# Optimization experiments

Hardware: AMD Instinct MI355X
Metric: run time of the kernel (lower is better)

## Reference

```python
import jax, jax.numpy as jnp
import numpy as np

CROP = 48
THRESHOLD = 0.5
IOU_THRESHOLD = 0.5


def _conv(x, w, b):
    # x: [N,H,W,C], w: [kh,kw,Cin,Cout]
    y = jax.lax.conv_general_dilated(x, w, (1, 1), 'VALID',
                                     dimension_numbers=('NHWC', 'HWIO', 'NHWC'))
    return y + b


def _prelu(x, a):
    # a broadcasts over the channel-last axis
    return jnp.where(x >= 0, x, a * x)


def _maxpool(x, k, s, p):
    return jax.lax.reduce_window(x, -jnp.inf, jax.lax.max,
                                 (1, k, k, 1), (1, s, s, 1),
                                 ((0, 0), (p, p), (p, p), (0, 0)))


def _nms_keep(boxes, scores, valid, iou_thr):
    # fixed-shape greedy NMS (torchvision semantics: suppress iou > thr)
    N = boxes.shape[0]
    s = jnp.where(valid, scores, -jnp.inf)
    order = jnp.argsort(-s)
    b = boxes[order]
    x1, y1, x2, y2 = b[:, 0], b[:, 1], b[:, 2], b[:, 3]
    area = (x2 - x1) * (y2 - y1)
    xx1 = jnp.maximum(x1[:, None], x1[None, :])
    yy1 = jnp.maximum(y1[:, None], y1[None, :])
    xx2 = jnp.minimum(x2[:, None], x2[None, :])
    yy2 = jnp.minimum(y2[:, None], y2[None, :])
    inter = jnp.clip(xx2 - xx1, 0.0) * jnp.clip(yy2 - yy1, 0.0)
    iou = inter / (area[:, None] + area[None, :] - inter + 1e-12)
    keep0 = valid[order]
    idx = jnp.arange(N)

    def body(i, keep):
        sup = (iou[i] > iou_thr) & (idx > i) & keep[i] & keep
        return keep & ~sup

    keep_sorted = jax.lax.fori_loop(0, N, body, keep0)
    return jnp.zeros(N, bool).at[order].set(keep_sorted)


def setup_inputs() -> dict:
    key = jax.random.key(0)
    ks = jax.random.split(key, 24)
    H = W = 1024
    N = 2048
    image = jax.random.uniform(ks[0], (H, W, 3), jnp.float32) * 255.0
    x1 = jax.random.uniform(ks[1], (N,), jnp.float32) * (W - 130)
    y1 = jax.random.uniform(ks[2], (N,), jnp.float32) * (H - 130)
    bw = 20.0 + jax.random.uniform(ks[3], (N,), jnp.float32) * 100.0
    bh = 20.0 + jax.random.uniform(ks[4], (N,), jnp.float32) * 100.0
    bboxes = jnp.stack([x1, y1, x1 + bw, y1 + bh], axis=1)
    rn = lambda k, sh, s: jax.random.normal(k, sh, jnp.float32) * s
    return {
        'bboxes': bboxes, 'image': image,
        'conv1_w': rn(ks[5], (3, 3, 3, 32), 0.05), 'conv1_b': rn(ks[6], (32,), 0.01),
        'prelu1': 0.25 * jnp.ones((32,), jnp.float32),
        'conv2_w': rn(ks[7], (3, 3, 32, 64), 0.05), 'conv2_b': rn(ks[8], (64,), 0.01),
        'prelu2': 0.25 * jnp.ones((64,), jnp.float32),
        'conv3_w': rn(ks[9], (3, 3, 64, 64), 0.05), 'conv3_b': rn(ks[10], (64,), 0.01),
        'prelu3': 0.25 * jnp.ones((64,), jnp.float32),
        'conv4_w': rn(ks[11], (2, 2, 64, 128), 0.05), 'conv4_b': rn(ks[12], (128,), 0.01),
        'prelu4': 0.25 * jnp.ones((128,), jnp.float32),
        'fc5_w': rn(ks[13], (256, 1152), 0.02), 'fc5_b': rn(ks[14], (256,), 0.01),
        'prelu5': 0.25 * jnp.ones((256,), jnp.float32),
        'fc6a_w': rn(ks[15], (2, 256), 0.1), 'fc6a_b': rn(ks[16], (2,), 0.01),
        'fc6b_w': rn(ks[17], (4, 256), 0.1), 'fc6b_b': rn(ks[18], (4,), 0.01),
    }


def reference(bboxes, image, conv1_w, conv1_b, prelu1, conv2_w, conv2_b, prelu2,
              conv3_w, conv3_b, prelu3, conv4_w, conv4_b, prelu4,
              fc5_w, fc5_b, prelu5, fc6a_w, fc6a_b, fc6b_w, fc6b_b):
    H, W = image.shape[0], image.shape[1]
    N = bboxes.shape[0]
    # preprocess (torch: (x - 127.5) * 0.0078125)
    data = (image - 127.5) * 0.0078125  # [H,W,3]
    # clip boxes in place like the torch forward
    bx1 = jnp.clip(bboxes[:, 0], 0.0, None)
    by1 = jnp.clip(bboxes[:, 1], 0.0, None)
    bx2 = jnp.clip(bboxes[:, 2], None, float(W))
    by2 = jnp.clip(bboxes[:, 3], None, float(H))
    bb = jnp.stack([bx1, by1, bx2, by2], axis=1)  # clipped boxes [N,4]
    # integer crop windows (torch .int() truncation; coords >= 0)
    ib = bb.astype(jnp.int32)
    cw = jnp.maximum(ib[:, 2] - ib[:, 0], 1)
    ch = jnp.maximum(ib[:, 3] - ib[:, 1], 1)
    # nearest-neighbor resize to 48x48 (F.interpolate default mode='nearest')
    r = jnp.arange(CROP, dtype=jnp.int32)
    xs = ib[:, 0:1] + (r[None, :] * cw[:, None]) // CROP  # [N,48]
    ys = ib[:, 1:2] + (r[None, :] * ch[:, None]) // CROP  # [N,48]
    crops = data[ys[:, :, None], xs[:, None, :], :]  # [N,48,48,3] gather
    # CNN trunk
    h = _maxpool(_prelu(_conv(crops, conv1_w, conv1_b), prelu1), 3, 2, 1)
    h = _maxpool(_prelu(_conv(h, conv2_w, conv2_b), prelu2), 3, 2, 0)
    h = _maxpool(_prelu(_conv(h, conv3_w, conv3_b), prelu3), 2, 2, 0)
    h = _prelu(_conv(h, conv4_w, conv4_b), prelu4)  # [N,3,3,128]
    h = jnp.transpose(h, (0, 3, 1, 2)).reshape(N, -1)  # NCHW flatten like torch -> [N,1152]
    h = _prelu(h @ fc5_w.T + fc5_b, prelu5)  # [N,256]
    cls = jax.nn.softmax(h @ fc6a_w.T + fc6a_b, axis=1)  # [N,2]
    reg = h @ fc6b_w.T + fc6b_b  # [N,4]
    score = cls[:, 1]
    valid = score >= THRESHOLD
    w = bb[:, 2] - bb[:, 0]
    hgt = bb[:, 3] - bb[:, 1]
    out = jnp.stack([bb[:, 0] + reg[:, 0] * w,
                     bb[:, 1] + reg[:, 1] * hgt,
                     bb[:, 2] + reg[:, 2] * w,
                     bb[:, 3] + reg[:, 3] * hgt], axis=1)  # [N,4]
    keep = _nms_keep(out, score, valid, IOU_THRESHOLD)
    return jnp.where(keep[:, None], out, 0.0)
```

## Files before the change

kernel.cpp:

```cpp
#include <hip/hip_runtime.h>
#include <math.h>
#include <stdint.h>

#define NBOX 2048

#define P1_RS 25
#define P1_CS 576
#define P1_SZ 18432

__device__ __forceinline__ void fma4(float4& a, float s, const float4& w) {
  a.x = fmaf(s, w.x, a.x); a.y = fmaf(s, w.y, a.y);
  a.z = fmaf(s, w.z, a.z); a.w = fmaf(s, w.w, a.w);
}
__device__ __forceinline__ float4 max4(float4 a, float4 b) {
  return make_float4(fmaxf(a.x,b.x), fmaxf(a.y,b.y), fmaxf(a.z,b.z), fmaxf(a.w,b.w));
}
__device__ __forceinline__ float4 max34(float4 a, float4 b, float4 c) {
  return max4(max4(a, b), c);
}
__device__ __forceinline__ float4 prelu4(float4 v, float4 a) {
  float4 r;
  r.x = v.x >= 0.f ? v.x : a.x*v.x;
  r.y = v.y >= 0.f ? v.y : a.y*v.y;
  r.z = v.z >= 0.f ? v.z : a.z*v.z;
  r.w = v.w >= 0.f ? v.w : a.w*v.w;
  return r;
}
__device__ __forceinline__ float4 shfl4(float4 v, int src) {
  float4 r;
  r.x = __shfl(v.x, src, 64); r.y = __shfl(v.y, src, 64);
  r.z = __shfl(v.z, src, 64); r.w = __shfl(v.w, src, 64);
  return r;
}

__global__ __launch_bounds__(256) void k1_crop_conv1(
    const float* __restrict__ bboxes, const float* __restrict__ image,
    const float* __restrict__ w1, const float* __restrict__ b1, const float* __restrict__ a1,
    float* __restrict__ p1ws, int box0)
{
  __shared__ float crop[48*48*3];
  const int tid = threadIdx.x;
  const int n = box0 + blockIdx.x;

  float f0 = bboxes[n*4+0], f1 = bboxes[n*4+1], f2 = bboxes[n*4+2], f3 = bboxes[n*4+3];
  float bx1 = fmaxf(f0, 0.f), by1 = fmaxf(f1, 0.f);
  float bx2 = fminf(f2, 1024.f), by2 = fminf(f3, 1024.f);
  int ix1 = (int)bx1, iy1 = (int)by1, ix2 = (int)bx2, iy2 = (int)by2;
  int cw = ix2 - ix1; if (cw < 1) cw = 1;
  int ch = iy2 - iy1; if (ch < 1) ch = 1;

  for (int idx = tid; idx < 6912; idx += 256) {
    int c = idx % 3; int t = idx / 3; int j = t % 48; int i = t / 48;
    int gx = ix1 + (j * cw) / 48;
    int gy = iy1 + (i * ch) / 48;
    float v = image[(gy*1024 + gx)*3 + c];
    crop[idx] = (v - 127.5f) * 0.0078125f;
  }
  __syncthreads();

  float* p1o = p1ws + (size_t)blockIdx.x * P1_SZ;

  for (int slot = tid; slot < 1104; slot += 256) {
    int cq = slot & 7;
    int t2 = slot >> 3;
    int pjq = t2 % 6;
    int pi  = t2 / 6;
    int pj0 = pjq * 4;
    int c0 = 2*pj0 - 1;
    float4 bias  = *(const float4*)&b1[cq*4];
    float4 alpha = *(const float4*)&a1[cq*4];
    float4 mx[4];
#pragma unroll
    for (int t = 0; t < 4; t++) mx[t] = make_float4(-3.0e38f,-3.0e38f,-3.0e38f,-3.0e38f);

#pragma unroll
    for (int dr = 0; dr < 3; dr++) {
      int r = 2*pi - 1 + dr;
      if (r < 0 || r > 45) continue;
      float4 acc[9];
#pragma unroll
      for (int c = 0; c < 9; c++) acc[c] = bias;
#pragma unroll
      for (int kh = 0; kh < 3; kh++) {
        int row = r + kh;
        float s[33];
#pragma unroll
        for (int d = 0; d < 11; d++) {
          int cc = c0 + d; cc = cc < 0 ? 0 : (cc > 47 ? 47 : cc);
          int base = row*144 + cc*3;
          s[d*3+0] = crop[base+0];
          s[d*3+1] = crop[base+1];
          s[d*3+2] = crop[base+2];
        }
#pragma unroll
        for (int kw = 0; kw < 3; kw++) {
#pragma unroll
          for (int ci = 0; ci < 3; ci++) {
            float4 w = *(const float4*)&w1[((kh*3+kw)*3+ci)*32 + cq*4];
#pragma unroll
            for (int c = 0; c < 9; c++) fma4(acc[c], s[(c+kw)*3+ci], w);
          }
        }
      }
#pragma unroll
      for (int c = 0; c < 9; c++) {
        int cabs = c0 + c;
        if (cabs < 0 || cabs > 45) continue;
        float4 pv = prelu4(acc[c], alpha);
#pragma unroll
        for (int t = 0; t < 4; t++) {
          if (c >= 2*t && c <= 2*t+2) mx[t] = max4(mx[t], pv);
        }
      }
    }
#pragma unroll
    for (int t = 0; t < 4; t++) {
      int pj = pj0 + t;
      if (pj < 23) {
        int base = pi*P1_RS + pj;
        p1o[(cq*4+0)*P1_CS + base] = mx[t].x;
        p1o[(cq*4+1)*P1_CS + base] = mx[t].y;
        p1o[(cq*4+2)*P1_CS + base] = mx[t].z;
        p1o[(cq*4+3)*P1_CS + base] = mx[t].w;
      }
    }
  }
}

#define K2_LOADW(W, CI, KH) { \
  const float* wp_ = w2 + (((KH)*3)*32 + (CI))*64 + co0; \
  W[0] = *(const float4*)(wp_);            W[1] = *(const float4*)(wp_ + 4); \
  W[2] = *(const float4*)(wp_ + 2048);     W[3] = *(const float4*)(wp_ + 2052); \
  W[4] = *(const float4*)(wp_ + 4096);     W[5] = *(const float4*)(wp_ + 4100); }

#define K2_COMP(W, CIL, KH) { \
  const float* ip_ = &in_s[(CIL)*P1_CS + (rl+(KH))*P1_RS + j0]; \
  float s_[9]; \
  _Pragma("unroll") for (int d_ = 0; d_ < 9; d_++) s_[d_] = ip_[d_]; \
  _Pragma("unroll") for (int kw_ = 0; kw_ < 3; kw_++) { \
    _Pragma("unroll") for (int jj_ = 0; jj_ < 7; jj_++) { \
      fma4(acc[jj_][0], s_[jj_+kw_], W[kw_*2]); \
      fma4(acc[jj_][1], s_[jj_+kw_], W[kw_*2+1]); } } }

#define K2_STORE8(PJ, LO, HI) { \
  float* d_ = p2o + (size_t)co0*120 + pi*12 + (PJ); \
  float4 lo_ = (LO), hi_ = (HI); \
  d_[0]   = lo_.x; d_[120] = lo_.y; d_[240] = lo_.z; d_[360] = lo_.w; \
  d_[480] = hi_.x; d_[600] = hi_.y; d_[720] = hi_.z; d_[840] = hi_.w; }

__global__ __launch_bounds__(512, 4) void k2_conv2(
    const float* __restrict__ w2, const float* __restrict__ b2, const float* __restrict__ a2,
    const float* __restrict__ p1ws, float* __restrict__ p2ws)
{
  __shared__ float in_s[9216];
  const int tid = threadIdx.x;
  const float* p1o = p1ws + (size_t)blockIdx.x * P1_SZ;
  float* p2o = p2ws + (size_t)blockIdx.x * 7680;

  const int wav = __builtin_amdgcn_readfirstlane(tid >> 6);
  const int lane = tid & 63;
  int jt = lane / 21;
  int rl = lane - jt * 21;
  if (lane == 63) { jt = 2; rl = 20; }
  const int j0 = jt * 7;
  const int co0 = wav * 8;

  float4 bL = *(const float4*)&b2[co0];
  float4 bH = *(const float4*)&b2[co0+4];
  float4 aL = *(const float4*)&a2[co0];
  float4 aH = *(const float4*)&a2[co0+4];

  float4 acc[7][2];
#pragma unroll
  for (int jj = 0; jj < 7; jj++) { acc[jj][0] = bL; acc[jj][1] = bH; }

#pragma unroll 1
  for (int h = 0; h < 2; h++) {
    __syncthreads();
    for (int i4 = tid; i4 < 2304; i4 += 512)
      *(float4*)&in_s[i4*4] = *(const float4*)&p1o[h*9216 + i4*4];
    __syncthreads();

    const int cb = h*16;
    float4 wA[6], wB[6];
    K2_LOADW(wA, cb+0, 0);
#pragma unroll 1
    for (int ci = 0; ci < 16; ci += 2) {
      K2_LOADW(wB, cb+ci, 1);
      K2_COMP(wA, ci, 0);
      K2_LOADW(wA, cb+ci, 2);
      K2_COMP(wB, ci, 1);
      K2_LOADW(wB, cb+ci+1, 0);
      K2_COMP(wA, ci, 2);
      K2_LOADW(wA, cb+ci+1, 1);
      K2_COMP(wB, ci+1, 0);
      K2_LOADW(wB, cb+ci+1, 2);
      K2_COMP(wA, ci+1, 1);
      if (ci + 2 < 16) K2_LOADW(wA, cb+ci+2, 0);
      K2_COMP(wB, ci+1, 2);
    }
  }

#pragma unroll
  for (int jj = 0; jj < 7; jj++) {
    acc[jj][0] = prelu4(acc[jj][0], aL);
    acc[jj][1] = prelu4(acc[jj][1], aH);
  }

#pragma unroll
  for (int jj = 0; jj < 7; jj++) {
#pragma unroll
    for (int h = 0; h < 2; h++) {
      float4 v = acc[jj][h];
      float4 d1 = shfl4(v, lane + 1);
      float4 d2 = shfl4(v, lane + 2);
      acc[jj][h] = max34(v, d1, d2);
    }
  }
  float4 r0[2], r1[2];
#pragma unroll
  for (int h = 0; h < 2; h++) {
    r0[h] = shfl4(acc[0][h], lane + 21);
    r1[h] = shfl4(acc[1][h], lane + 21);
  }

  if (((rl & 1) == 0) && rl <= 18) {
    const int pi = rl >> 1;
    if (jt == 0) {
      K2_STORE8(0, max34(acc[0][0],acc[1][0],acc[2][0]), max34(acc[0][1],acc[1][1],acc[2][1]));
      K2_STORE8(1, max34(acc[2][0],acc[3][0],acc[4][0]), max34(acc[2][1],acc[3][1],acc[4][1]));
      K2_STORE8(2, max34(acc[4][0],acc[5][0],acc[6][0]), max34(acc[4][1],acc[5][1],acc[6][1]));
      K2_STORE8(3, max34(acc[6][0],r0[0],r1[0]),          max34(acc[6][1],r0[1],r1[1]));
    } else if (jt == 1) {
      K2_STORE8(4, max34(acc[1][0],acc[2][0],acc[3][0]), max34(acc[1][1],acc[2][1],acc[3][1]));
      K2_STORE8(5, max34(acc[3][0],acc[4][0],acc[5][0]), max34(acc[3][1],acc[4][1],acc[5][1]));
      K2_STORE8(6, max34(acc[5][0],acc[6][0],r0[0]),     max34(acc[5][1],acc[6][1],r0[1]));
    } else {
      K2_STORE8(7, max34(acc[0][0],acc[1][0],acc[2][0]), max34(acc[0][1],acc[1][1],acc[2][1]));
      K2_STORE8(8, max34(acc[2][0],acc[3][0],acc[4][0]), max34(acc[2][1],acc[3][1],acc[4][1]));
      K2_STORE8(9, max34(acc[4][0],acc[5][0],acc[6][0]), max34(acc[4][1],acc[5][1],acc[6][1]));
    }
  }
}

#define K3_LOADW(W, CI, KH) { \
  const float* wp_ = w3 + (((KH)*3)*64 + (CI))*64 + co0; \
  W[0] = *(const float4*)(wp_);            W[1] = *(const float4*)(wp_ + 4); \
  W[2] = *(const float4*)(wp_ + 4096);     W[3] = *(const float4*)(wp_ + 4100); \
  W[4] = *(const float4*)(wp_ + 8192);     W[5] = *(const float4*)(wp_ + 8196); }

#define K3_COMP(W, CIL, KH) { \
  const float* ip_ = ibase + (CIL)*120 + (KH)*12; \
  float2 sA_ = *(const float2*)(ip_); \
  float2 sB_ = *(const float2*)(ip_ + 2); \
  float s_[4] = {sA_.x, sA_.y, sB_.x, sB_.y}; \
  _Pragma("unroll") for (int kw_ = 0; kw_ < 3; kw_++) { \
    _Pragma("unroll") for (int c_ = 0; c_ < 2; c_++) { \
      fma4(acc[c_][0], s_[c_+kw_], W[kw_*2]); \
      fma4(acc[c_][1], s_[c_+kw_], W[kw_*2+1]); } } }

__global__ __launch_bounds__(512, 4) void k3_conv3(
    const float* __restrict__ w3, const float* __restrict__ b3, const float* __restrict__ a3,
    const float* __restrict__ p2ws, float* __restrict__ p3ws)
{
  __shared__ float in_s[7696];
  const int tid = threadIdx.x;
  const float* p2o = p2ws + (size_t)(blockIdx.x*2) * 7680;
  float* p3o0 = p3ws + (size_t)(blockIdx.x*2) * 1024;

  const int wav = __builtin_amdgcn_readfirstlane(tid >> 6);
  const int lane = tid & 63;
  const int b  = lane >> 5;
  const int r  = (lane >> 2) & 7;
  const int cg = lane & 3;
  const int co0 = wav * 8;

  float4 bL = *(const float4*)&b3[co0];
  float4 bH = *(const float4*)&b3[co0+4];
  float4 aL = *(const float4*)&a3[co0];
  float4 aH = *(const float4*)&a3[co0+4];

  float4 acc[2][2];
  acc[0][0] = bL; acc[0][1] = bH; acc[1][0] = bL; acc[1][1] = bH;

  const float* ibase = &in_s[b*3848 + r*12 + cg*2];

#pragma unroll 1
  for (int h = 0; h < 2; h++) {
    __syncthreads();
    for (int i4 = tid; i4 < 1920; i4 += 512) {
      int bb = (i4 >= 960) ? 1 : 0;
      int k = i4 - bb*960;
      *(float4*)&in_s[bb*3848 + k*4] = *(const float4*)&p2o[(size_t)bb*7680 + h*3840 + k*4];
    }
    __syncthreads();

    const int cb = h*32;
    float4 wA[6], wB[6];
    K3_LOADW(wA, cb+0, 0);
#pragma unroll 1
    for (int ci = 0; ci < 32; ci += 2) {
      K3_LOADW(wB, cb+ci, 1);
      K3_COMP(wA, ci, 0);
      K3_LOADW(wA, cb+ci, 2);
      K3_COMP(wB, ci, 1);
      K3_LOADW(wB, cb+ci+1, 0);
      K3_COMP(wA, ci, 2);
      K3_LOADW(wA, cb+ci+1, 1);
      K3_COMP(wB, ci+1, 0);
      K3_LOADW(wB, cb+ci+1, 2);
      K3_COMP(wA, ci+1, 1);
      if (ci + 2 < 32) K3_LOADW(wA, cb+ci+2, 0);
      K3_COMP(wB, ci+1, 2);
    }
  }

  float4 hm[2];
#pragma unroll
  for (int h = 0; h < 2; h++) {
    float4 p0 = prelu4(acc[0][h], h ? aH : aL);
    float4 p1 = prelu4(acc[1][h], h ? aH : aL);
    hm[h] = max4(p0, p1);
  }
  float4 o[2];
#pragma unroll
  for (int h = 0; h < 2; h++) {
    float4 d = shfl4(hm[h], lane + 4);
    o[h] = max4(hm[h], d);
  }
  if ((r & 1) == 0) {
    const int pi = r >> 1;
    float* d = p3o0 + b*1024 + (size_t)co0*16 + pi*4 + cg;
    d[0]   = o[0].x; d[16]  = o[0].y; d[32]  = o[0].z; d[48]  = o[0].w;
    d[64]  = o[1].x; d[80]  = o[1].y; d[96]  = o[1].z; d[112] = o[1].w;
  }
}

#define K4_LOADW(W, CI) { \
  const float* wp_ = w4 + (CI)*128 + co0; \
  W[0] = *(const float4*)(wp_);           W[1] = *(const float4*)(wp_ + 4); \
  W[2] = *(const float4*)(wp_ + 8192);    W[3] = *(const float4*)(wp_ + 8196); \
  W[4] = *(const float4*)(wp_ + 16384);   W[5] = *(const float4*)(wp_ + 16388); \
  W[6] = *(const float4*)(wp_ + 24576);   W[7] = *(const float4*)(wp_ + 24580); }

#define K4_COMP(W, CI) { \
  const float* ip_ = base + (CI)*16; \
  float i00 = ip_[0], i01 = ip_[1], i10 = ip_[4], i11 = ip_[5]; \
  fma4(acc0, i00, W[0]); fma4(acc1, i00, W[1]); \
  fma4(acc0, i01, W[2]); fma4(acc1, i01, W[3]); \
  fma4(acc0, i10, W[4]); fma4(acc1, i10, W[5]); \
  fma4(acc0, i11, W[6]); fma4(acc1, i11, W[7]); }

__global__ __launch_bounds__(512) void k4_conv4(
    const float* __restrict__ w4, const float* __restrict__ b4, const float* __restrict__ a4,
    const float* __restrict__ p3ws, float* __restrict__ c4ws)
{
  __shared__ float p3s[4*1032];
  const int tid = threadIdx.x;
  const int bi0 = blockIdx.x * 4;

  for (int i4 = tid; i4 < 1024; i4 += 512) {
    int bb = i4 >> 8, k = i4 & 255;
    *(float4*)&p3s[bb*1032 + k*4] = *(const float4*)&p3ws[(size_t)(bi0+bb)*1024 + k*4];
  }
  __syncthreads();

  const int wav = __builtin_amdgcn_readfirstlane(tid >> 6);
  const int lane = tid & 63;
  const int bx = lane >> 4;
  const int sp = lane & 15;
  const bool act = sp < 9;
  const int sq = act ? sp : 8;
  const int r = sq / 3, c = sq - 3*r;
  const float* base = &p3s[bx*1032 + r*4 + c];
  float* c4o = c4ws + (size_t)(bi0+bx)*1152;

#pragma unroll 1
  for (int p = 0; p < 2; p++) {
    const int co0 = p*64 + wav*8;
    float4 bL = *(const float4*)&b4[co0];
    float4 bH = *(const float4*)&b4[co0+4];
    float4 aL = *(const float4*)&a4[co0];
    float4 aH = *(const float4*)&a4[co0+4];
    float4 acc0 = bL, acc1 = bH;

    float4 wA[8], wB[8];
    K4_LOADW(wA, 0);
#pragma unroll 1
    for (int ci = 0; ci < 64; ci += 2) {
      K4_LOADW(wB, ci+1);
      K4_COMP(wA, ci);
      if (ci + 2 < 64) K4_LOADW(wA, ci+2);
      K4_COMP(wB, ci+1);
    }

    if (act) {
      float4 p0 = prelu4(acc0, aL);
      float4 p1 = prelu4(acc1, aH);
      float* d = c4o + (size_t)co0*9 + sp;
      d[0]  = p0.x; d[9]  = p0.y; d[18] = p0.z; d[27] = p0.w;
      d[36] = p1.x; d[45] = p1.y; d[54] = p1.z; d[63] = p1.w;
    }
  }
}

__global__ __launch_bounds__(512) void k5_fc(
    const float* __restrict__ fc5w, const float* __restrict__ fc5b, const float* __restrict__ a5,
    const float* __restrict__ w6a, const float* __restrict__ b6a,
    const float* __restrict__ w6b, const float* __restrict__ b6b,
    const float* __restrict__ bboxes, const float* __restrict__ c4ws,
    float* __restrict__ ws_scores, float* __restrict__ ws_boxes, int box0)
{
  __shared__ float c4s[8*1152];
  __shared__ float hs[8*256];
  __shared__ float l6[8][6];
  const int tid = threadIdx.x;
  const int lb0 = blockIdx.x * 8;
  for (int idx4 = tid; idx4 < 2304; idx4 += 512)
    *(float4*)&c4s[idx4*4] = *(const float4*)&c4ws[(size_t)lb0*1152 + idx4*4];
  __syncthreads();

  const int wav = __builtin_amdgcn_readfirstlane(tid >> 6);
  const int lane = tid & 63;
  const int half = lane >> 5;
  const int l32  = lane & 31;
  const int b    = 2*(wav & 3) + half;
  const int ob   = (wav >> 2) * 128;
  const float* cb = &c4s[b*1152 + l32*4];

#pragma unroll 1
  for (int oi = 0; oi < 128; oi++) {
    const int o = ob + oi;
    const float* wr = fc5w + (size_t)o*1152 + l32*4;
    float acc = 0.f;
#pragma unroll
    for (int j = 0; j < 9; j++) {
      float4 wv = *(const float4*)(wr + j*128);
      float4 cv = *(const float4*)(cb + j*128);
      acc = fmaf(cv.x, wv.x, acc);
      acc = fmaf(cv.y, wv.y, acc);
      acc = fmaf(cv.z, wv.z, acc);
      acc = fmaf(cv.w, wv.w, acc);
    }
    acc += __shfl_down(acc, 16, 32);
    acc += __shfl_down(acc,  8, 32);
    acc += __shfl_down(acc,  4, 32);
    acc += __shfl_down(acc,  2, 32);
    acc += __shfl_down(acc,  1, 32);
    if (l32 == 0) {
      float h = acc + fc5b[o];
      h = h >= 0.f ? h : a5[o]*h;
      hs[b*256 + o] = h;
    }
  }
  __syncthreads();

  if (tid < 48) {
    int bb = tid / 6, oi = tid % 6;
    const float* w = (oi < 2) ? &w6a[oi*256] : &w6b[(oi-2)*256];
    float d = (oi < 2) ? b6a[oi] : b6b[oi-2];
    const float* hh = &hs[bb*256];
    for (int k = 0; k < 256; k++) d += hh[k]*w[k];
    l6[bb][oi] = d;
  }
  __syncthreads();
  if (tid < 8) {
    int n = box0 + lb0 + tid;
    float l0 = l6[tid][0], l1 = l6[tid][1];
    float m = fmaxf(l0, l1);
    float e0 = expf(l0-m), e1 = expf(l1-m);
    float score = e1/(e0+e1);
    float r0 = l6[tid][2], r1 = l6[tid][3], r2 = l6[tid][4], r3 = l6[tid][5];
    float f0 = bboxes[n*4+0], f1 = bboxes[n*4+1], f2 = bboxes[n*4+2], f3 = bboxes[n*4+3];
    float bx1 = fmaxf(f0, 0.f), by1 = fmaxf(f1, 0.f);
    float bx2 = fminf(f2, 1024.f), by2 = fminf(f3, 1024.f);
    float w_ = bx2-bx1, h_ = by2-by1;
    ws_scores[n] = score;
    float4 ob2 = make_float4(bx1 + r0*w_, by1 + r1*h_, bx2 + r2*w_, by2 + r3*h_);
    *(float4*)&ws_boxes[n*4] = ob2;
  }
}

__global__ __launch_bounds__(1024) void k6a_sort(
    const float* __restrict__ ws_scores, const float* __restrict__ ws_boxes,
    int* __restrict__ sidx_ws, float* __restrict__ sbox_ws,
    float* __restrict__ area_ws, int* __restrict__ nv_ws)
{
  __shared__ float skey[2048];
  __shared__ int   sidx[2048];
  const int tid = threadIdx.x;
  for (int i = tid; i < 2048; i += 1024) {
    float s = ws_scores[i];
    skey[i] = (s >= 0.5f) ? s : -INFINITY;
    sidx[i] = i;
  }
  __syncthreads();
  for (int k = 2; k <= 2048; k <<= 1) {
    for (int j = k >> 1; j > 0; j >>= 1) {
      for (int i = tid; i < 2048; i += 1024) {
        int ixj = i ^ j;
        if (ixj > i) {
          float a = skey[i], b = skey[ixj];
          int ia = sidx[i], ib = sidx[ixj];
          bool up = ((i & k) == 0);
          bool aAfterB = (a < b) || (a == b && ia > ib);
          if (up ? aAfterB : !aAfterB) {
            skey[i] = b; skey[ixj] = a; sidx[i] = ib; sidx[ixj] = ia;
          }
        }
      }
      __syncthreads();
    }
  }
  if (tid == 0) nv_ws[0] = 2048;
  __syncthreads();
  for (int i = tid; i < 2048; i += 1024) {
    if (skey[i] == -INFINITY && (i == 0 || skey[i-1] != -INFINITY)) nv_ws[0] = i;
    int n = sidx[i];
    sidx_ws[i] = n;
    float4 b = *(const float4*)&ws_boxes[n*4];
    *(float4*)&sbox_ws[i*4] = b;
    area_ws[i] = (b.z-b.x)*(b.w-b.y);
  }
}

__global__ __launch_bounds__(256) void k6b_iou(
    const int* __restrict__ nv_ws, const float* __restrict__ sbox_ws,
    const float* __restrict__ area_ws, unsigned long long* __restrict__ M)
{
  const int nv = nv_ws[0];
  int gt = blockIdx.x*256 + threadIdx.x;
  for (int w = gt; w < 2048*32; w += 128*256) {
    int i = w >> 5, wg = w & 31;
    if (i >= nv) continue;
    float4 bi = *(const float4*)&sbox_ws[i*4];
    float ai = area_ws[i];
    unsigned long long m = 0;
    int jbase = wg*64;
    if (jbase + 63 > i) {
      for (int jj = 0; jj < 64; jj++) {
        int j = jbase + jj;
        if (j <= i) continue;
        float4 bj = *(const float4*)&sbox_ws[j*4];
        float xx1 = fmaxf(bi.x, bj.x), yy1 = fmaxf(bi.y, bj.y);
        float xx2 = fminf(bi.z, bj.z), yy2 = fminf(bi.w, bj.w);
        float iw = fmaxf(xx2-xx1, 0.f), ih = fmaxf(yy2-yy1, 0.f);
        float inter = iw*ih;
        float iou = inter / (ai + area_ws[j] - inter + 1e-12f);
        if (iou > 0.5f) m |= (1ull << jj);
      }
    }
    M[w] = m;
  }
}

__global__ __launch_bounds__(1024) void k6c_scan(
    const int* __restrict__ nv_ws, const int* __restrict__ sidx_ws,
    const float* __restrict__ sbox_ws, const unsigned long long* __restrict__ M,
    float* __restrict__ out)
{
  __shared__ unsigned long long Msh[128*32];
  __shared__ unsigned long long rem_sh[32];
  const int tid = threadIdx.x;
  const int nv = nv_ws[0];
  unsigned long long rem = 0;

  for (int c0 = 0; c0 < 2048; c0 += 128) {
    if (c0 >= nv) break;
    for (int w = tid; w < 128*32; w += 1024) {
      int i = c0 + (w >> 5);
      if (i < nv) Msh[w] = M[(size_t)i*32 + (w & 31)];
    }
    __syncthreads();
    if (tid < 64) {
      int iend = c0 + 128; if (iend > nv) iend = nv;
      for (int i = c0; i < iend; i += 4) {
        unsigned long long m0=0, m1=0, m2=0, m3=0;
        int base = (i - c0) << 5;
        if (tid < 32) {
          m0 = Msh[base + tid];
          if (i+1 < iend) m1 = Msh[base + 32 + tid];
          if (i+2 < iend) m2 = Msh[base + 64 + tid];
          if (i+3 < iend) m3 = Msh[base + 96 + tid];
        }
        unsigned long long rw = __shfl(rem, (i >> 6), 64);
        if (!((rw >> (i & 63)) & 1ull)) rem |= m0;
        if (i+1 < iend) {
          rw = __shfl(rem, ((i+1) >> 6), 64);
          if (!((rw >> ((i+1) & 63)) & 1ull)) rem |= m1;
        }
        if (i+2 < iend) {
          rw = __shfl(rem, ((i+2) >> 6), 64);
          if (!((rw >> ((i+2) & 63)) & 1ull)) rem |= m2;
        }
        if (i+3 < iend) {
          rw = __shfl(rem, ((i+3) >> 6), 64);
          if (!((rw >> ((i+3) & 63)) & 1ull)) rem |= m3;
        }
      }
    }
    __syncthreads();
  }
  if (tid < 32) rem_sh[tid] = rem;
  __syncthreads();
  for (int i = tid; i < 2048; i += 1024) {
    bool keep = (i < nv) && !((rem_sh[i >> 6] >> (i & 63)) & 1ull);
    int n = sidx_ws[i];
    float4 b = *(const float4*)&sbox_ws[i*4];
    float4 o = keep ? b : make_float4(0.f,0.f,0.f,0.f);
    *(float4*)&out[n*4] = o;
  }
}

extern "C" void kernel_launch(void* const* d_in, const int* in_sizes, int n_in,
                              void* d_out, int out_size, void* d_ws, size_t ws_size,
                              hipStream_t stream)
{
  const float* bboxes = (const float*)d_in[0];
  const float* image  = (const float*)d_in[1];
  const float* w1 = (const float*)d_in[2];  const float* b1 = (const float*)d_in[3];  const float* a1 = (const float*)d_in[4];
  const float* w2 = (const float*)d_in[5];  const float* b2 = (const float*)d_in[6];  const float* a2 = (const float*)d_in[7];
  const float* w3 = (const float*)d_in[8];  const float* b3 = (const float*)d_in[9];  const float* a3 = (const float*)d_in[10];
  const float* w4 = (const float*)d_in[11]; const float* b4 = (const float*)d_in[12]; const float* a4 = (const float*)d_in[13];
  const float* fc5w = (const float*)d_in[14]; const float* fc5b = (const float*)d_in[15]; const float* a5 = (const float*)d_in[16];
  const float* w6a = (const float*)d_in[17]; const float* b6a = (const float*)d_in[18];
  const float* w6b = (const float*)d_in[19]; const float* b6b = (const float*)d_in[20];
  float* out = (float*)d_out;

  char* ws = (char*)d_ws;
  size_t off = 0;
  auto alloc = [&](size_t bytes) -> size_t {
    size_t p = off; off += (bytes + 255) & ~(size_t)255; return p;
  };
  size_t o_scores = alloc(NBOX*4);
  size_t o_boxes  = alloc(NBOX*16);
  size_t o_sidx   = alloc(NBOX*4);
  size_t o_sbox   = alloc(NBOX*16);
  size_t o_area   = alloc(NBOX*4);
  size_t o_nv     = alloc(256);
  size_t o_M      = alloc((size_t)NBOX*32*8);
  size_t fixed = off;
  const size_t perbox = (size_t)(P1_SZ + 7680 + 1024 + 1152) * 4;

  int B = NBOX;
  if (fixed + (size_t)B*perbox > ws_size) {
    size_t avail = ws_size > fixed ? ws_size - fixed : 0;
    B = (int)(avail / perbox);
    B &= ~7;
    if (B < 8) B = 8;
    if (B > NBOX) B = NBOX;
  }
  size_t o_p1 = alloc((size_t)B*P1_SZ*4);
  size_t o_p2 = alloc((size_t)B*7680*4);
  size_t o_p3 = alloc((size_t)B*1024*4);
  size_t o_c4 = alloc((size_t)B*1152*4);

  float* ws_scores = (float*)(ws + o_scores);
  float* ws_boxes  = (float*)(ws + o_boxes);
  int*   sidxp     = (int*)(ws + o_sidx);
  float* sboxp     = (float*)(ws + o_sbox);
  float* areap     = (float*)(ws + o_area);
  int*   nvp       = (int*)(ws + o_nv);
  unsigned long long* Mp = (unsigned long long*)(ws + o_M);
  float* p1p = (float*)(ws + o_p1);
  float* p2p = (float*)(ws + o_p2);
  float* p3p = (float*)(ws + o_p3);
  float* c4p = (float*)(ws + o_c4);

  for (int c0 = 0; c0 < NBOX; c0 += B) {
    int Bc = NBOX - c0; if (Bc > B) Bc = B;
    k1_crop_conv1<<<Bc, 256, 0, stream>>>(bboxes, image, w1, b1, a1, p1p, c0);
    k2_conv2<<<Bc, 512, 0, stream>>>(w2, b2, a2, p1p, p2p);
    k3_conv3<<<Bc/2, 512, 0, stream>>>(w3, b3, a3, p2p, p3p);
    k4_conv4<<<Bc/4, 512, 0, stream>>>(w4, b4, a4, p3p, c4p);
    k5_fc<<<Bc/8, 512, 0, stream>>>(fc5w, fc5b, a5, w6a, b6a, w6b, b6b,
                                    bboxes, c4p, ws_scores, ws_boxes, c0);
  }
  k6a_sort<<<1, 1024, 0, stream>>>(ws_scores, ws_boxes, sidxp, sboxp, areap, nvp);
  k6b_iou<<<128, 256, 0, stream>>>(nvp, sboxp, areap, Mp);
  k6c_scan<<<1, 1024, 0, stream>>>(nvp, sidxp, sboxp, Mp, out);
}
```

Measured before the change: 1.552 ms.

## Fuse conv3 and conv4 kernels via shared memory, widen conv1 block, unroll fc5

Merges the conv3 and conv4 kernels so the pooled conv3 output stays in shared memory instead of round-tripping through a global workspace, and remaps conv4 work so each wave handles 32 output channels for one box. conv1 blocks grow to 512 threads, and the fc5 loop computes two outputs per iteration to reuse the activation loads. In exchange, the fused kernel drops the __launch_bounds__ occupancy hint and the conv4 weight prefetch double-buffering, and each block processes only 2 boxes in conv4 instead of 4.

```diff
diff --git a/kernel.cpp b/kernel.cpp
--- a/kernel.cpp
+++ b/kernel.cpp
@@ -33,7 +33,7 @@
   return r;
 }
 
-__global__ __launch_bounds__(256) void k1_crop_conv1(
+__global__ __launch_bounds__(512) void k1_crop_conv1(
     const float* __restrict__ bboxes, const float* __restrict__ image,
     const float* __restrict__ w1, const float* __restrict__ b1, const float* __restrict__ a1,
     float* __restrict__ p1ws, int box0)
@@ -49,7 +49,7 @@
   int cw = ix2 - ix1; if (cw < 1) cw = 1;
   int ch = iy2 - iy1; if (ch < 1) ch = 1;
 
-  for (int idx = tid; idx < 6912; idx += 256) {
+  for (int idx = tid; idx < 6912; idx += 512) {
     int c = idx % 3; int t = idx / 3; int j = t % 48; int i = t / 48;
     int gx = ix1 + (j * cw) / 48;
     int gy = iy1 + (i * ch) / 48;
@@ -60,7 +60,7 @@
 
   float* p1o = p1ws + (size_t)blockIdx.x * P1_SZ;
 
-  for (int slot = tid; slot < 1104; slot += 256) {
+  for (int slot = tid; slot < 1104; slot += 512) {
     int cq = slot & 7;
     int t2 = slot >> 3;
     int pjq = t2 % 6;
@@ -259,145 +259,120 @@
       fma4(acc[c_][0], s_[c_+kw_], W[kw_*2]); \
       fma4(acc[c_][1], s_[c_+kw_], W[kw_*2+1]); } } }
 
-__global__ __launch_bounds__(512, 4) void k3_conv3(
+__global__ __launch_bounds__(512) void k34_conv34(
     const float* __restrict__ w3, const float* __restrict__ b3, const float* __restrict__ a3,
-    const float* __restrict__ p2ws, float* __restrict__ p3ws)
+    const float* __restrict__ w4, const float* __restrict__ b4, const float* __restrict__ a4,
+    const float* __restrict__ p2ws, float* __restrict__ c4ws)
 {
   __shared__ float in_s[7696];
+  __shared__ float p3s[2*1032];
   const int tid = threadIdx.x;
-  const float* p2o = p2ws + (size_t)(blockIdx.x*2) * 7680;
-  float* p3o0 = p3ws + (size_t)(blockIdx.x*2) * 1024;
+  const int bi0 = blockIdx.x * 2;
+  const float* p2o = p2ws + (size_t)bi0 * 7680;
 
   const int wav = __builtin_amdgcn_readfirstlane(tid >> 6);
   const int lane = tid & 63;
-  const int b  = lane >> 5;
-  const int r  = (lane >> 2) & 7;
-  const int cg = lane & 3;
-  const int co0 = wav * 8;
-
-  float4 bL = *(const float4*)&b3[co0];
-  float4 bH = *(const float4*)&b3[co0+4];
-  float4 aL = *(const float4*)&a3[co0];
-  float4 aH = *(const float4*)&a3[co0+4];
-
-  float4 acc[2][2];
-  acc[0][0] = bL; acc[0][1] = bH; acc[1][0] = bL; acc[1][1] = bH;
-
-  const float* ibase = &in_s[b*3848 + r*12 + cg*2];
+
+  {
+    const int b  = lane >> 5;
+    const int r  = (lane >> 2) & 7;
+    const int cg = lane & 3;
+    const int co0 = wav * 8;
+
+    float4 bL = *(const float4*)&b3[co0];
+    float4 bH = *(const float4*)&b3[co0+4];
+    float4 aL = *(const float4*)&a3[co0];
+    float4 aH = *(const float4*)&a3[co0+4];
+
+    float4 acc[2][2];
+    acc[0][0] = bL; acc[0][1] = bH; acc[1][0] = bL; acc[1][1] = bH;
+
+    const float* ibase = &in_s[b*3848 + r*12 + cg*2];
 
 #pragma unroll 1
-  for (int h = 0; h < 2; h++) {
-    __syncthreads();
-    for (int i4 = tid; i4 < 1920; i4 += 512) {
-      int bb = (i4 >= 960) ? 1 : 0;
-      int k = i4 - bb*960;
-      *(float4*)&in_s[bb*3848 + k*4] = *(const float4*)&p2o[(size_t)bb*7680 + h*3840 + k*4];
-    }
-    __syncthreads();
-
-    const int cb = h*32;
-    float4 wA[6], wB[6];
-    K3_LOADW(wA, cb+0, 0);
+    for (int h = 0; h < 2; h++) {
+      __syncthreads();
+      for (int i4 = tid; i4 < 1920; i4 += 512) {
+        int bb = (i4 >= 960) ? 1 : 0;
+        int k = i4 - bb*960;
+        *(float4*)&in_s[bb*3848 + k*4] = *(const float4*)&p2o[(size_t)bb*7680 + h*3840 + k*4];
+      }
+      __syncthreads();
+
+      const int cb = h*32;
+      float4 wA[6], wB[6];
+      K3_LOADW(wA, cb+0, 0);
 #pragma unroll 1
-    for (int ci = 0; ci < 32; ci += 2) {
-      K3_LOADW(wB, cb+ci, 1);
-      K3_COMP(wA, ci, 0);
-      K3_LOADW(wA, cb+ci, 2);
-      K3_COMP(wB, ci, 1);
-      K3_LOADW(wB, cb+ci+1, 0);
-      K3_COMP(wA, ci, 2);
-      K3_LOADW(wA, cb+ci+1, 1);
-      K3_COMP(wB, ci+1, 0);
-      K3_LOADW(wB, cb+ci+1, 2);
-      K3_COMP(wA, ci+1, 1);
-      if (ci + 2 < 32) K3_LOADW(wA, cb+ci+2, 0);
-      K3_COMP(wB, ci+1, 2);
-    }
-  }
-
-  float4 hm[2];
-#pragma unroll
-  for (int h = 0; h < 2; h++) {
-    float4 p0 = prelu4(acc[0][h], h ? aH : aL);
-    float4 p1 = prelu4(acc[1][h], h ? aH : aL);
-    hm[h] = max4(p0, p1);
-  }
-  float4 o[2];
-#pragma unroll
-  for (int h = 0; h < 2; h++) {
-    float4 d = shfl4(hm[h], lane + 4);
-    o[h] = max4(hm[h], d);
-  }
-  if ((r & 1) == 0) {
-    const int pi = r >> 1;
-    float* d = p3o0 + b*1024 + (size_t)co0*16 + pi*4 + cg;
-    d[0]   = o[0].x; d[16]  = o[0].y; d[32]  = o[0].z; d[48]  = o[0].w;
-    d[64]  = o[1].x; d[80]  = o[1].y; d[96]  = o[1].z; d[112] = o[1].w;
-  }
-}
-
-#define K4_LOADW(W, CI) { \
-  const float* wp_ = w4 + (CI)*128 + co0; \
-  W[0] = *(const float4*)(wp_);           W[1] = *(const float4*)(wp_ + 4); \
-  W[2] = *(const float4*)(wp_ + 8192);    W[3] = *(const float4*)(wp_ + 8196); \
-  W[4] = *(const float4*)(wp_ + 16384);   W[5] = *(const float4*)(wp_ + 16388); \
-  W[6] = *(const float4*)(wp_ + 24576);   W[7] = *(const float4*)(wp_ + 24580); }
-
-#define K4_COMP(W, CI) { \
-  const float* ip_ = base + (CI)*16; \
-  float i00 = ip_[0], i01 = ip_[1], i10 = ip_[4], i11 = ip_[5]; \
-  fma4(acc0, i00, W[0]); fma4(acc1, i00, W[1]); \
-  fma4(acc0, i01, W[2]); fma4(acc1, i01, W[3]); \
-  fma4(acc0, i10, W[4]); fma4(acc1, i10, W[5]); \
-  fma4(acc0, i11, W[6]); fma4(acc1, i11, W[7]); }
-
-__global__ __launch_bounds__(512) void k4_conv4(
-    const float* __restrict__ w4, const float* __restrict__ b4, const float* __restrict__ a4,
-    const float* __restrict__ p3ws, float* __restrict__ c4ws)
-{
-  __shared__ float p3s[4*1032];
-  const int tid = threadIdx.x;
-  const int bi0 = blockIdx.x * 4;
-
-  for (int i4 = tid; i4 < 1024; i4 += 512) {
-    int bb = i4 >> 8, k = i4 & 255;
-    *(float4*)&p3s[bb*1032 + k*4] = *(const float4*)&p3ws[(size_t)(bi0+bb)*1024 + k*4];
-  }
-  __syncthreads();
-
-  const int wav = __builtin_amdgcn_readfirstlane(tid >> 6);
-  const int lane = tid & 63;
-  const int bx = lane >> 4;
-  const int sp = lane & 15;
-  const bool act = sp < 9;
-  const int sq = act ? sp : 8;
-  const int r = sq / 3, c = sq - 3*r;
-  const float* base = &p3s[bx*1032 + r*4 + c];
-  float* c4o = c4ws + (size_t)(bi0+bx)*1152;
-
+      for (int ci = 0; ci < 32; ci += 2) {
+        K3_LOADW(wB, cb+ci, 1);
+        K3_COMP(wA, ci, 0);
+        K3_LOADW(wA, cb+ci, 2);
+        K3_COMP(wB, ci, 1);
+        K3_LOADW(wB, cb+ci+1, 0);
+        K3_COMP(wA, ci, 2);
+        K3_LOADW(wA, cb+ci+1, 1);
+        K3_COMP(wB, ci+1, 0);
+        K3_LOADW(wB, cb+ci+1, 2);
+        K3_COMP(wA, ci+1, 1);
+        if (ci + 2 < 32) K3_LOADW(wA, cb+ci+2, 0);
+        K3_COMP(wB, ci+1, 2);
+      }
+    }
+
+    float4 hm[2];
+#pragma unroll
+    for (int h = 0; h < 2; h++) {
+      float4 p0 = prelu4(acc[0][h], h ? aH : aL);
+      float4 p1 = prelu4(acc[1][h], h ? aH : aL);
+      hm[h] = max4(p0, p1);
+    }
+    float4 o[2];
+#pragma unroll
+    for (int h = 0; h < 2; h++) {
+      float4 d = shfl4(hm[h], lane + 4);
+      o[h] = max4(hm[h], d);
+    }
+    if ((r & 1) == 0) {
+      const int pi = r >> 1;
+      float* d = &p3s[b*1032 + co0*16 + pi*4 + cg];
+      d[0]   = o[0].x; d[16]  = o[0].y; d[32]  = o[0].z; d[48]  = o[0].w;
+      d[64]  = o[1].x; d[80]  = o[1].y; d[96]  = o[1].z; d[112] = o[1].w;
+    }
+  }
+  __syncthreads();
+
+  {
+    const int bb  = wav >> 2;
+    const int wv  = wav & 3;
+    const int coq = lane >> 4;
+    const int sp  = lane & 15;
+    const bool act = sp < 9;
+    const int sq = act ? sp : 8;
+    const int r4 = sq / 3, cc4 = sq - 3*r4;
+    const int co8 = wv*32 + coq*8;
+    const float* base = &p3s[bb*1032 + r4*4 + cc4];
+    float* c4o = c4ws + (size_t)(bi0+bb)*1152;
+
+    float4 acc0 = *(const float4*)&b4[co8];
+    float4 acc1 = *(const float4*)&b4[co8+4];
 #pragma unroll 1
-  for (int p = 0; p < 2; p++) {
-    const int co0 = p*64 + wav*8;
-    float4 bL = *(const float4*)&b4[co0];
-    float4 bH = *(const float4*)&b4[co0+4];
-    float4 aL = *(const float4*)&a4[co0];
-    float4 aH = *(const float4*)&a4[co0+4];
-    float4 acc0 = bL, acc1 = bH;
-
-    float4 wA[8], wB[8];
-    K4_LOADW(wA, 0);
-#pragma unroll 1
-    for (int ci = 0; ci < 64; ci += 2) {
-      K4_LOADW(wB, ci+1);
-      K4_COMP(wA, ci);
-      if (ci + 2 < 64) K4_LOADW(wA, ci+2);
-      K4_COMP(wB, ci+1);
-    }
-
+    for (int ci = 0; ci < 64; ci++) {
+      const float* ip = base + ci*16;
+      float i00 = ip[0], i01 = ip[1], i10 = ip[4], i11 = ip[5];
+      const float* wp = w4 + ci*128 + co8;
+      float4 W00a = *(const float4*)(wp);         float4 W00b = *(const float4*)(wp+4);
+      float4 W01a = *(const float4*)(wp + 8192);  float4 W01b = *(const float4*)(wp+8196);
+      float4 W10a = *(const float4*)(wp + 16384); float4 W10b = *(const float4*)(wp+16388);
+      float4 W11a = *(const float4*)(wp + 24576); float4 W11b = *(const float4*)(wp+24580);
+      fma4(acc0, i00, W00a); fma4(acc1, i00, W00b);
+      fma4(acc0, i01, W01a); fma4(acc1, i01, W01b);
+      fma4(acc0, i10, W10a); fma4(acc1, i10, W10b);
+      fma4(acc0, i11, W11a); fma4(acc1, i11, W11b);
+    }
     if (act) {
-      float4 p0 = prelu4(acc0, aL);
-      float4 p1 = prelu4(acc1, aH);
-      float* d = c4o + (size_t)co0*9 + sp;
+      float4 p0 = prelu4(acc0, *(const float4*)&a4[co8]);
+      float4 p1 = prelu4(acc1, *(const float4*)&a4[co8+4]);
+      float* d = c4o + (size_t)co8*9 + sp;
       d[0]  = p0.x; d[9]  = p0.y; d[18] = p0.z; d[27] = p0.w;
       d[36] = p1.x; d[45] = p1.y; d[54] = p1.z; d[63] = p1.w;
     }
@@ -429,28 +404,33 @@
   const float* cb = &c4s[b*1152 + l32*4];
 
 #pragma unroll 1
-  for (int oi = 0; oi < 128; oi++) {
-    const int o = ob + oi;
-    const float* wr = fc5w + (size_t)o*1152 + l32*4;
-    float acc = 0.f;
+  for (int oi = 0; oi < 128; oi += 2) {
+    const int o0 = ob + oi, o1 = ob + oi + 1;
+    const float* wr0 = fc5w + (size_t)o0*1152 + l32*4;
+    const float* wr1 = wr0 + 1152;
+    float ac0 = 0.f, ac1 = 0.f;
 #pragma unroll
     for (int j = 0; j < 9; j++) {
-      float4 wv = *(const float4*)(wr + j*128);
       float4 cv = *(const float4*)(cb + j*128);
-      acc = fmaf(cv.x, wv.x, acc);
-      acc = fmaf(cv.y, wv.y, acc);
-      acc = fmaf(cv.z, wv.z, acc);
-      acc = fmaf(cv.w, wv.w, acc);
-    }
-    acc += __shfl_down(acc, 16, 32);
-    acc += __shfl_down(acc,  8, 32);
-    acc += __shfl_down(acc,  4, 32);
-    acc += __shfl_down(acc,  2, 32);
-    acc += __shfl_down(acc,  1, 32);
+      float4 w0 = *(const float4*)(wr0 + j*128);
+      float4 w1v = *(const float4*)(wr1 + j*128);
+      ac0 = fmaf(cv.x, w0.x, ac0);  ac1 = fmaf(cv.x, w1v.x, ac1);
+      ac0 = fmaf(cv.y, w0.y, ac0);  ac1 = fmaf(cv.y, w1v.y, ac1);
+      ac0 = fmaf(cv.z, w0.z, ac0);  ac1 = fmaf(cv.z, w1v.z, ac1);
+      ac0 = fmaf(cv.w, w0.w, ac0);  ac1 = fmaf(cv.w, w1v.w, ac1);
+    }
+    ac0 += __shfl_down(ac0, 16, 32);  ac1 += __shfl_down(ac1, 16, 32);
+    ac0 += __shfl_down(ac0,  8, 32);  ac1 += __shfl_down(ac1,  8, 32);
+    ac0 += __shfl_down(ac0,  4, 32);  ac1 += __shfl_down(ac1,  4, 32);
+    ac0 += __shfl_down(ac0,  2, 32);  ac1 += __shfl_down(ac1,  2, 32);
+    ac0 += __shfl_down(ac0,  1, 32);  ac1 += __shfl_down(ac1,  1, 32);
     if (l32 == 0) {
-      float h = acc + fc5b[o];
-      h = h >= 0.f ? h : a5[o]*h;
-      hs[b*256 + o] = h;
+      float h0 = ac0 + fc5b[o0];
+      h0 = h0 >= 0.f ? h0 : a5[o0]*h0;
+      hs[b*256 + o0] = h0;
+      float h1 = ac1 + fc5b[o1];
+      h1 = h1 >= 0.f ? h1 : a5[o1]*h1;
+      hs[b*256 + o1] = h1;
     }
   }
   __syncthreads();
@@ -640,7 +620,7 @@
   size_t o_nv     = alloc(256);
   size_t o_M      = alloc((size_t)NBOX*32*8);
   size_t fixed = off;
-  const size_t perbox = (size_t)(P1_SZ + 7680 + 1024 + 1152) * 4;
+  const size_t perbox = (size_t)(P1_SZ + 7680 + 1152) * 4;
 
   int B = NBOX;
   if (fixed + (size_t)B*perbox > ws_size) {
@@ -652,7 +632,6 @@
   }
   size_t o_p1 = alloc((size_t)B*P1_SZ*4);
   size_t o_p2 = alloc((size_t)B*7680*4);
-  size_t o_p3 = alloc((size_t)B*1024*4);
   size_t o_c4 = alloc((size_t)B*1152*4);
 
   float* ws_scores = (float*)(ws + o_scores);
@@ -664,15 +643,13 @@
   unsigned long long* Mp = (unsigned long long*)(ws + o_M);
   float* p1p = (float*)(ws + o_p1);
   float* p2p = (float*)(ws + o_p2);
-  float* p3p = (float*)(ws + o_p3);
   float* c4p = (float*)(ws + o_c4);
 
   for (int c0 = 0; c0 < NBOX; c0 += B) {
     int Bc = NBOX - c0; if (Bc > B) Bc = B;
-    k1_crop_conv1<<<Bc, 256, 0, stream>>>(bboxes, image, w1, b1, a1, p1p, c0);
+    k1_crop_conv1<<<Bc, 512, 0, stream>>>(bboxes, image, w1, b1, a1, p1p, c0);
     k2_conv2<<<Bc, 512, 0, stream>>>(w2, b2, a2, p1p, p2p);
-    k3_conv3<<<Bc/2, 512, 0, stream>>>(w3, b3, a3, p2p, p3p);
-    k4_conv4<<<Bc/4, 512, 0, stream>>>(w4, b4, a4, p3p, c4p);
+    k34_conv34<<<Bc/2, 512, 0, stream>>>(w3, b3, a3, w4, b4, a4, p2p, c4p);
     k5_fc<<<Bc/8, 512, 0, stream>>>(fc5w, fc5b, a5, w6a, b6a, w6b, b6b,
                                     bboxes, c4p, ws_scores, ws_boxes, c0);
   }
```

Measured after the change: 2.418 ms. 55.8% more time.
